# Optimization experiments

Hardware: AMD Instinct MI355X
Metric: run time of the kernel (lower is better)

Reference implementation:

```python
import jax, jax.numpy as jnp
import numpy as np

B, S, H, D = 4, 2048, 16, 64
E = H * D  # embedding_dim = 1024


def setup_inputs() -> dict:
    key = jax.random.key(0)
    ks = jax.random.split(key, 5)
    scale = 1.0 / np.sqrt(E)
    return {
        "x": jax.random.normal(ks[0], (B, S, E), dtype=jnp.float32),
        "wq": jax.random.normal(ks[1], (E, E), dtype=jnp.float32) * scale,
        "wk": jax.random.normal(ks[2], (E, E), dtype=jnp.float32) * scale,
        "wv": jax.random.normal(ks[3], (E, E), dtype=jnp.float32) * scale,
        "wo": jax.random.normal(ks[4], (E, E), dtype=jnp.float32) * scale,
    }


def reference(x, wq, wk, wv, wo):
    b, s, e = x.shape
    # nn.Linear: y = x @ W^T (no bias; use_bias=False)
    q = (x @ wq.T).reshape(b, s, H, D)
    k = (x @ wk.T).reshape(b, s, H, D)
    v = (x @ wv.T).reshape(b, s, H, D)
    # NOTE: original scales by sqrt(embedding_dim), not sqrt(head_dim)
    scores = jnp.einsum("bqhd,bkhd->bhqk", q, k) / jnp.sqrt(jnp.float32(e))
    causal = jnp.tril(jnp.ones((s, s), dtype=bool))  # mask[:s,:s]
    scores = jnp.where(causal, scores, -jnp.inf)
    attn = jax.nn.softmax(scores, axis=-1)
    out = jnp.einsum("bhql,blhd->bqhd", attn, v).reshape(b, s, e)
    return out @ wo.T
```

## Files before the change

### kernel.cpp

```cpp
#include <hip/hip_runtime.h>
#include <hip/hip_bf16.h>

#define E_DIM 1024
#define NHEAD 16
#define HDIM  64
#define BATCH 4
#define SEQ   2048
#define RQKV  (3 * E_DIM)

typedef __attribute__((ext_vector_type(8))) short bf16x8;
typedef __attribute__((ext_vector_type(4))) float f32x4;
typedef __attribute__((ext_vector_type(16))) float f32x16;

#define SCL2 0.04508422f

static __device__ __forceinline__ unsigned short bits_of(__hip_bfloat16 h) {
    return *reinterpret_cast<unsigned short*>(&h);
}

static __device__ __forceinline__ void gload_lds16(const void* g, void* l) {
    __builtin_amdgcn_global_load_lds(
        (__attribute__((address_space(1))) void*)g,
        (__attribute__((address_space(3))) void*)l, 16, 0, 0);
}

static __device__ __forceinline__ unsigned cvt_pk_bf16(float a, float b) {
    unsigned r;
    asm("v_cvt_pk_bf16_f32 %0, %1, %2" : "=v"(r) : "v"(a), "v"(b));
    return r;
}

static __device__ __forceinline__ float exp2_raw(float x) {
    float r;
    asm("v_exp_f32 %0, %1" : "=v"(r) : "v"(x));
    return r;
}

__global__ void cast_all_kernel(
    const float* __restrict__ x,  const float* __restrict__ wq,
    const float* __restrict__ wk, const float* __restrict__ wv,
    const float* __restrict__ wo,
    __hip_bfloat16* __restrict__ xb, __hip_bfloat16* __restrict__ wqkvb,
    __hip_bfloat16* __restrict__ wob) {
    const int NX4 = (BATCH * SEQ * E_DIM) / 4;
    const int NW4 = (E_DIM * E_DIM) / 4;
    int id = blockIdx.x * 256 + threadIdx.x;

    const float* in;
    __hip_bfloat16* out;
    float scl = 1.0f;
    if (id < NX4) {
        in = x; out = xb;
    } else {
        const int r = id - NX4;
        const int wsel = r >> 18;
        id = r & (NW4 - 1);
        switch (wsel) {
            case 0: in = wq; out = wqkvb;            scl = SCL2; break;
            case 1: in = wk; out = wqkvb + NW4 * 4;  break;
            case 2: in = wv; out = wqkvb + NW4 * 8;  break;
            default: in = wo; out = wob;             break;
        }
    }
    float4 v = reinterpret_cast<const float4*>(in)[id];
    ushort4 u;
    u.x = bits_of(__float2bfloat16(v.x * scl));
    u.y = bits_of(__float2bfloat16(v.y * scl));
    u.z = bits_of(__float2bfloat16(v.z * scl));
    u.w = bits_of(__float2bfloat16(v.w * scl));
    reinterpret_cast<ushort4*>(out)[id] = u;
}

template<int FN, int OUT_F32>
__global__ __launch_bounds__(512) void gemm_ph(
    const __hip_bfloat16* __restrict__ A,
    const __hip_bfloat16* __restrict__ Bw,
    void* __restrict__ Cv,
    int M, int N, int K) {
    constexpr int BN = FN * 64;
    __shared__ __align__(16) __hip_bfloat16 As[2][128 * 64];
    __shared__ __align__(16) __hip_bfloat16 Bs[2][BN * 64];

    const int nbx = gridDim.x;
    const int lin = blockIdx.y * nbx + blockIdx.x;
    const int cpx = (nbx * gridDim.y) >> 3;
    const int swz = (lin & 7) * cpx + (lin >> 3);
    const int mBase = (swz / nbx) * 128, nBase = (swz % nbx) * BN;

    const int t = threadIdx.x, lane = t & 63, w = t >> 6;
    const int wr = w >> 2, wc = w & 3;
    const int lr = lane & 15;
    const int lkb = (lane >> 4) * 16;

    f32x4 acc[4][FN];
#pragma unroll
    for (int i = 0; i < 4; ++i)
#pragma unroll
        for (int j = 0; j < FN; ++j) acc[i][j] = (f32x4){0.f, 0.f, 0.f, 0.f};

    const int NKT = K >> 6;

    auto STAGE = [&](int kt, int b) {
#pragma unroll
        for (int i = 0; i < 2; ++i) {
            const int q = i * 512 + t;
            const int r = q >> 3, cb = (q & 7) * 16;
            const char* src = (const char*)A +
                ((size_t)(mBase + r) * K + kt * 64) * 2 + (cb ^ ((r & 7) << 4));
            gload_lds16(src, (char*)&As[b][0] + q * 16);
        }
#pragma unroll
        for (int i = 0; i < FN; ++i) {
            const int q = i * 512 + t;
            const int r = q >> 3, cb = (q & 7) * 16;
            const char* src = (const char*)Bw +
                ((size_t)(nBase + r) * K + kt * 64) * 2 + (cb ^ ((r & 7) << 4));
            gload_lds16(src, (char*)&Bs[b][0] + q * 16);
        }
    };

    STAGE(0, 0);
    for (int kt = 0; kt < NKT; ++kt) {
        const int buf = kt & 1;
        asm volatile("s_waitcnt vmcnt(0)" ::: "memory");
        __builtin_amdgcn_s_barrier();
        __builtin_amdgcn_sched_barrier(0);

        bf16x8 bfr[FN][2];
        {
#pragma unroll
            for (int fn = 0; fn < FN; ++fn)
#pragma unroll
                for (int ks = 0; ks < 2; ++ks) {
                    const int R = wc * (FN * 16) + fn * 16 + lr;
                    const int addr = R * 128 + ((ks * 64 + lkb) ^ ((R & 7) << 4));
                    bfr[fn][ks] = *reinterpret_cast<const bf16x8*>(
                        (const char*)&Bs[buf][0] + addr);
                }
            bf16x8 af[2][2];
#pragma unroll
            for (int f = 0; f < 2; ++f)
#pragma unroll
                for (int ks = 0; ks < 2; ++ks) {
                    const int R = wr * 64 + f * 16 + lr;
                    const int addr = R * 128 + ((ks * 64 + lkb) ^ ((R & 7) << 4));
                    af[f][ks] = *reinterpret_cast<const bf16x8*>(
                        (const char*)&As[buf][0] + addr);
                }
            if (kt + 1 < NKT) STAGE(kt + 1, buf ^ 1);
            asm volatile("s_waitcnt lgkmcnt(0)" ::: "memory");
            __builtin_amdgcn_sched_barrier(0);
            __builtin_amdgcn_s_setprio(1);
#pragma unroll
            for (int f = 0; f < 2; ++f)
#pragma unroll
                for (int fn = 0; fn < FN; ++fn)
#pragma unroll
                    for (int ks = 0; ks < 2; ++ks)
                        acc[f][fn] = __builtin_amdgcn_mfma_f32_16x16x32_bf16(
                            af[f][ks], bfr[fn][ks], acc[f][fn], 0, 0, 0);
            __builtin_amdgcn_s_setprio(0);
            __builtin_amdgcn_s_barrier();
        }
        {
            bf16x8 af[2][2];
#pragma unroll
            for (int f = 0; f < 2; ++f)
#pragma unroll
                for (int ks = 0; ks < 2; ++ks) {
                    const int R = wr * 64 + (f + 2) * 16 + lr;
                    const int addr = R * 128 + ((ks * 64 + lkb) ^ ((R & 7) << 4));
                    af[f][ks] = *reinterpret_cast<const bf16x8*>(
                        (const char*)&As[buf][0] + addr);
                }
            asm volatile("s_waitcnt lgkmcnt(0)" ::: "memory");
            __builtin_amdgcn_sched_barrier(0);
            __builtin_amdgcn_s_setprio(1);
#pragma unroll
            for (int f = 0; f < 2; ++f)
#pragma unroll
                for (int fn = 0; fn < FN; ++fn)
#pragma unroll
                    for (int ks = 0; ks < 2; ++ks)
                        acc[f + 2][fn] = __builtin_amdgcn_mfma_f32_16x16x32_bf16(
                            af[f][ks], bfr[fn][ks], acc[f + 2][fn], 0, 0, 0);
            __builtin_amdgcn_s_setprio(0);
        }
    }

#pragma unroll
    for (int fm = 0; fm < 4; ++fm)
#pragma unroll
        for (int fn = 0; fn < FN; ++fn)
#pragma unroll
            for (int v = 0; v < 4; ++v) {
                const int row = mBase + wr * 64 + fm * 16 + (lane >> 4) * 4 + v;
                const int col = nBase + wc * (FN * 16) + fn * 16 + lr;
                if (OUT_F32)
                    ((float*)Cv)[(size_t)row * N + col] = acc[fm][fn][v];
                else
                    ((__hip_bfloat16*)Cv)[(size_t)row * N + col] =
                        __float2bfloat16(acc[fm][fn][v]);
            }
}

__global__ __launch_bounds__(256) void attn_kernel(
    const __hip_bfloat16* __restrict__ QKV,
    __hip_bfloat16* __restrict__ O) {
    __shared__ __align__(16) __hip_bfloat16 Kl[2][64][64];
    __shared__ __align__(16) __hip_bfloat16 Vt[2][64][64];

    const int t = threadIdx.x, w = t >> 6, lane = t & 63;
    const int lq = lane & 31, hi = lane >> 5;

    const int id = blockIdx.x;
    const int c = id & 7, k = id >> 3;
    const int bh = (k & 7) * 8 + c;
    const int qq = k >> 3;
    const int qb = (qq & 4) ? (qq < 8 ? qq + 4 : qq - 12) : 15 - qq;
    const int b = bh >> 4, h = bh & 15;

    const size_t rb = (size_t)b * SEQ;
    const __hip_bfloat16* Qg = QKV + rb * RQKV + h * HDIM;
    const __hip_bfloat16* Kg = QKV + rb * RQKV + E_DIM + h * HDIM;
    const __hip_bfloat16* Vg = QKV + rb * RQKV + 2 * E_DIM + h * HDIM;

    const int kst_row  = w * 16 + (lane >> 3);
    const int kst_slot = lane & 7;
    const int vkp = t & 31, vd0 = (t >> 5) * 8;

    const int qw0 = qb * 128 + w * 32;
    const int qg  = qw0 + lq;

    bf16x8 aq[4];
#pragma unroll
    for (int d0 = 0; d0 < 4; ++d0)
        aq[d0] = *reinterpret_cast<const bf16x8*>(
            Qg + (size_t)qg * RQKV + d0 * 16 + hi * 8);

    f32x16 oa[2];
#pragma unroll
    for (int m = 0; m < 2; ++m)
#pragma unroll
        for (int r = 0; r < 16; ++r) oa[m][r] = 0.f;
    float l_run = 0.f;

    const int NP = qb + 1;
    for (int pr = 0; pr < NP; ++pr) {
        const int k0a = pr * 128;
        __syncthreads();

#pragma unroll
        for (int half = 0; half < 2; ++half)
#pragma unroll
            for (int i = 0; i < 2; ++i) {
                const int r = kst_row + i * 8;
                const char* src =
                    (const char*)(Kg + (size_t)(k0a + half * 64 + r) * RQKV) +
                    ((kst_slot * 16) ^ ((r & 7) << 4));
                gload_lds16(src, &Kl[half][w * 16 + i * 8][0]);
            }
        {
            const __hip_bfloat16* vp0 =
                Vg + (size_t)(k0a + 2 * vkp) * RQKV + vd0;
            const __hip_bfloat16* vp1 = vp0 + (size_t)64 * RQKV;
            union { bf16x8 v; unsigned u[4]; } A0, B0, A1, B1;
            A0.v = *reinterpret_cast<const bf16x8*>(vp0);
            B0.v = *reinterpret_cast<const bf16x8*>(vp0 + RQKV);
            A1.v = *reinterpret_cast<const bf16x8*>(vp1);
            B1.v = *reinterpret_cast<const bf16x8*>(vp1 + RQKV);
            char* vt0 = reinterpret_cast<char*>(&Vt[0][0][0]);
            char* vt1 = reinterpret_cast<char*>(&Vt[1][0][0]);
#pragma unroll
            for (int jw = 0; jw < 4; ++jw) {
                const int da = vd0 + 2 * jw, db = da + 1;
                const int offa = da * 128 + ((vkp * 4) ^ ((da & 7) << 4));
                const int offb = db * 128 + ((vkp * 4) ^ ((db & 7) << 4));
                *reinterpret_cast<unsigned*>(vt0 + offa) =
                    __builtin_amdgcn_perm(B0.u[jw], A0.u[jw], 0x05040100u);
                *reinterpret_cast<unsigned*>(vt0 + offb) =
                    __builtin_amdgcn_perm(B0.u[jw], A0.u[jw], 0x07060302u);
                *reinterpret_cast<unsigned*>(vt1 + offa) =
                    __builtin_amdgcn_perm(B1.u[jw], A1.u[jw], 0x05040100u);
                *reinterpret_cast<unsigned*>(vt1 + offb) =
                    __builtin_amdgcn_perm(B1.u[jw], A1.u[jw], 0x07060302u);
            }
        }
        __syncthreads();

#pragma unroll
        for (int half = 0; half < 2; ++half) {
            const int k0 = k0a + half * 64;
            if (k0 > qw0 + 31) continue;

            f32x16 sc2[2];
            const char* klbase = (const char*)&Kl[half][0][0];
#pragma unroll
            for (int tt = 0; tt < 2; ++tt) {
#pragma unroll
                for (int r = 0; r < 16; ++r) sc2[tt][r] = 0.f;
                const int kr = tt * 32 + lq;
                const char* kbase = klbase + kr * 128;
                const int swz = (kr & 7) << 4;
#pragma unroll
                for (int d0 = 0; d0 < 4; ++d0) {
                    bf16x8 ak = *reinterpret_cast<const bf16x8*>(
                        kbase + ((d0 * 32 + hi * 16) ^ swz));
                    sc2[tt] = __builtin_amdgcn_mfma_f32_32x32x16_bf16(
                        ak, aq[d0], sc2[tt], 0, 0, 0);
                }
            }
            if (k0 + 63 > qw0) {
#pragma unroll
                for (int tt = 0; tt < 2; ++tt)
#pragma unroll
                    for (int r = 0; r < 16; ++r) {
                        const int kgl = k0 + tt * 32 +
                                        (r & 3) + 8 * (r >> 2) + 4 * hi;
                        if (kgl > qg) sc2[tt][r] = -1e30f;
                    }
            }
            float rsum = 0.f;
#pragma unroll
            for (int tt = 0; tt < 2; ++tt) {
                float s0 = 0.f, s1 = 0.f, s2 = 0.f, s3 = 0.f;
#pragma unroll
                for (int r = 0; r < 16; r += 4) {
                    float p0 = exp2_raw(sc2[tt][r]);
                    float p1 = exp2_raw(sc2[tt][r + 1]);
                    float p2 = exp2_raw(sc2[tt][r + 2]);
                    float p3 = exp2_raw(sc2[tt][r + 3]);
                    sc2[tt][r] = p0; sc2[tt][r + 1] = p1;
                    sc2[tt][r + 2] = p2; sc2[tt][r + 3] = p3;
                    s0 += p0; s1 += p1; s2 += p2; s3 += p3;
                }
                rsum += (s0 + s1) + (s2 + s3);
            }
            rsum += __shfl_xor(rsum, 32);
            l_run += rsum;

            const char* vtbase = (const char*)&Vt[half][0][0];
#pragma unroll
            for (int tt = 0; tt < 2; ++tt)
#pragma unroll
                for (int sl = 0; sl < 2; ++sl) {
                    const int rbs = sl * 8;
                    const unsigned wA = cvt_pk_bf16(sc2[tt][rbs + 0], sc2[tt][rbs + 1]);
                    const unsigned wB = cvt_pk_bf16(sc2[tt][rbs + 2], sc2[tt][rbs + 3]);
                    const unsigned wC = cvt_pk_bf16(sc2[tt][rbs + 4], sc2[tt][rbs + 5]);
                    const unsigned wD = cvt_pk_bf16(sc2[tt][rbs + 6], sc2[tt][rbs + 7]);
                    const auto pA = __builtin_amdgcn_permlane32_swap(wA, wC, false, false);
                    const auto pB = __builtin_amdgcn_permlane32_swap(wB, wD, false, false);
                    union { unsigned u[4]; bf16x8 v; } pf;
                    pf.u[0] = pA[0]; pf.u[1] = pB[0];
                    pf.u[2] = pA[1]; pf.u[3] = pB[1];
                    const int ks = tt * 2 + sl;
#pragma unroll
                    for (int m = 0; m < 2; ++m) {
                        const int dr = m * 32 + lq;
                        bf16x8 av = *reinterpret_cast<const bf16x8*>(
                            vtbase + dr * 128 +
                            ((ks * 32 + hi * 16) ^ ((dr & 7) << 4)));
                        oa[m] = __builtin_amdgcn_mfma_f32_32x32x16_bf16(
                            av, pf.v, oa[m], 0, 0, 0);
                    }
                }
        }
    }

    const float inv = 1.f / l_run;
    __hip_bfloat16* Orow = O + (rb + qg) * E_DIM + h * HDIM;
#pragma unroll
    for (int m = 0; m < 2; ++m)
#pragma unroll
        for (int q4 = 0; q4 < 4; ++q4) {
            ushort4 pk;
            pk.x = bits_of(__float2bfloat16(oa[m][q4 * 4 + 0] * inv));
            pk.y = bits_of(__float2bfloat16(oa[m][q4 * 4 + 1] * inv));
            pk.z = bits_of(__float2bfloat16(oa[m][q4 * 4 + 2] * inv));
            pk.w = bits_of(__float2bfloat16(oa[m][q4 * 4 + 3] * inv));
            *reinterpret_cast<ushort4*>(Orow + m * 32 + q4 * 8 + 4 * hi) = pk;
        }
}

extern "C" void kernel_launch(void* const* d_in, const int* in_sizes, int n_in,
                              void* d_out, int out_size, void* d_ws, size_t ws_size,
                              hipStream_t stream) {
    const float* x  = (const float*)d_in[0];
    const float* wq = (const float*)d_in[1];
    const float* wk = (const float*)d_in[2];
    const float* wv = (const float*)d_in[3];
    const float* wo = (const float*)d_in[4];

    const size_t SZ_X = (size_t)BATCH * SEQ * E_DIM;
    const size_t SZ_W = (size_t)E_DIM * E_DIM;

    char* p = (char*)d_ws;
    __hip_bfloat16* xb    = (__hip_bfloat16*)p; p += SZ_X * 2;
    __hip_bfloat16* wqkvb = (__hip_bfloat16*)p; p += 3 * SZ_W * 2;
    __hip_bfloat16* wob   = (__hip_bfloat16*)p; p += SZ_W * 2;
    __hip_bfloat16* QKVb  = (__hip_bfloat16*)p; p += SZ_X * 3 * 2;
    __hip_bfloat16* attb  = (__hip_bfloat16*)p; p += SZ_X * 2;

    cast_all_kernel<<<dim3(12288), 256, 0, stream>>>(
        x, wq, wk, wv, wo, xb, wqkvb, wob);

    const int M = BATCH * SEQ;
    gemm_ph<3, 0><<<dim3(RQKV / 192, M / 128), 512, 0, stream>>>(
        xb, wqkvb, QKVb, M, RQKV, E_DIM);

    attn_kernel<<<dim3(1024), 256, 0, stream>>>(QKVb, attb);

    gemm_ph<2, 1><<<dim3(E_DIM / 128, M / 128), 512, 0, stream>>>(
        attb, wob, d_out, M, E_DIM, E_DIM);
}
```

Measured before the change: 151.7 us.

## Split long causal query blocks across two KV halves and combine partials

Query tiles 8–15, which have the longest causal KV ranges, are each split into two work items. Each item covers half of the KV pairs and writes unnormalized fp32 partial outputs and row sums to workspace. A new combine kernel adds the two partials, normalizes, and writes bf16. This is meant to shorten the longest blocks and improve load balance across the grid. The cost is an extra kernel launch plus roughly 33 MB of fp32 partials written and read back. The plain summing of partials relies on softmax using no running max.

```diff
diff --git a/kernel.cpp b/kernel.cpp
--- a/kernel.cpp
+++ b/kernel.cpp
@@ -206,7 +206,9 @@
 
 __global__ __launch_bounds__(256) void attn_kernel(
     const __hip_bfloat16* __restrict__ QKV,
-    __hip_bfloat16* __restrict__ O) {
+    __hip_bfloat16* __restrict__ O,
+    float* __restrict__ Po,
+    float* __restrict__ Pl) {
     __shared__ __align__(16) __hip_bfloat16 Kl[2][64][64];
     __shared__ __align__(16) __hip_bfloat16 Vt[2][64][64];
 
@@ -214,11 +216,23 @@
     const int lq = lane & 31, hi = lane >> 5;
 
     const int id = blockIdx.x;
-    const int c = id & 7, k = id >> 3;
-    const int bh = (k & 7) * 8 + c;
-    const int qq = k >> 3;
-    const int qb = (qq & 4) ? (qq < 8 ? qq + 4 : qq - 12) : 15 - qq;
+    const int c = id & 7, j = id >> 3;
+    const int bh = (j & 7) * 8 + c;
+    const int job = j >> 3;
     const int b = bh >> 4, h = bh & 15;
+
+    int qb, prS, prE, sIdx = 0;
+    const bool split = (job >= 8);
+    if (!split) {
+        qb = job; prS = 0; prE = qb + 1;
+    } else {
+        const int qt = (job - 8) >> 1;
+        sIdx = (job - 8) & 1;
+        qb = 8 + qt;
+        const int h0 = (qb + 2) >> 1;
+        prS = sIdx ? h0 : 0;
+        prE = sIdx ? qb + 1 : h0;
+    }
 
     const size_t rb = (size_t)b * SEQ;
     const __hip_bfloat16* Qg = QKV + rb * RQKV + h * HDIM;
@@ -245,8 +259,7 @@
         for (int r = 0; r < 16; ++r) oa[m][r] = 0.f;
     float l_run = 0.f;
 
-    const int NP = qb + 1;
-    for (int pr = 0; pr < NP; ++pr) {
+    for (int pr = prS; pr < prE; ++pr) {
         const int k0a = pr * 128;
         __syncthreads();
 
@@ -368,19 +381,72 @@
         }
     }
 
-    const float inv = 1.f / l_run;
-    __hip_bfloat16* Orow = O + (rb + qg) * E_DIM + h * HDIM;
-#pragma unroll
-    for (int m = 0; m < 2; ++m)
-#pragma unroll
-        for (int q4 = 0; q4 < 4; ++q4) {
-            ushort4 pk;
-            pk.x = bits_of(__float2bfloat16(oa[m][q4 * 4 + 0] * inv));
-            pk.y = bits_of(__float2bfloat16(oa[m][q4 * 4 + 1] * inv));
-            pk.z = bits_of(__float2bfloat16(oa[m][q4 * 4 + 2] * inv));
-            pk.w = bits_of(__float2bfloat16(oa[m][q4 * 4 + 3] * inv));
-            *reinterpret_cast<ushort4*>(Orow + m * 32 + q4 * 8 + 4 * hi) = pk;
-        }
+    if (!split) {
+        const float inv = 1.f / l_run;
+        __hip_bfloat16* Orow = O + (rb + qg) * E_DIM + h * HDIM;
+#pragma unroll
+        for (int m = 0; m < 2; ++m)
+#pragma unroll
+            for (int q4 = 0; q4 < 4; ++q4) {
+                ushort4 pk;
+                pk.x = bits_of(__float2bfloat16(oa[m][q4 * 4 + 0] * inv));
+                pk.y = bits_of(__float2bfloat16(oa[m][q4 * 4 + 1] * inv));
+                pk.z = bits_of(__float2bfloat16(oa[m][q4 * 4 + 2] * inv));
+                pk.w = bits_of(__float2bfloat16(oa[m][q4 * 4 + 3] * inv));
+                *reinterpret_cast<ushort4*>(Orow + m * 32 + q4 * 8 + 4 * hi) = pk;
+            }
+    } else {
+        const int bhqt = bh * 8 + (qb - 8);
+        const int qlocal = w * 32 + lq;
+        float* Pr = Po + ((size_t)(bhqt * 2 + sIdx) * 128 + qlocal) * 64;
+#pragma unroll
+        for (int m = 0; m < 2; ++m)
+#pragma unroll
+            for (int q4 = 0; q4 < 4; ++q4) {
+                float4 st = {oa[m][q4 * 4 + 0], oa[m][q4 * 4 + 1],
+                             oa[m][q4 * 4 + 2], oa[m][q4 * 4 + 3]};
+                *reinterpret_cast<float4*>(Pr + m * 32 + q4 * 8 + 4 * hi) = st;
+            }
+        if (hi == 0)
+            Pl[(size_t)bhqt * 256 + sIdx * 128 + qlocal] = l_run;
+    }
+}
+
+__global__ __launch_bounds__(256) void combine_kernel(
+    const float* __restrict__ Po, const float* __restrict__ Pl,
+    __hip_bfloat16* __restrict__ O) {
+    const int g = blockIdx.x * 256 + threadIdx.x;
+    const int row = g >> 3, oct = g & 7;
+    const int ql = row & 127, bhqt = row >> 7;
+    const int qt = bhqt & 7, bh = bhqt >> 3;
+    const int b = bh >> 4, h = bh & 15;
+    const int qb = 8 + qt;
+
+    const float l = Pl[(size_t)bhqt * 256 + ql] +
+                    Pl[(size_t)bhqt * 256 + 128 + ql];
+    const float inv = 1.f / l;
+
+    const size_t a0 = ((size_t)(bhqt * 2) * 128 + ql) * 64 + oct * 8;
+    const size_t a1 = a0 + 128 * 64;
+    const float4 p0a = *reinterpret_cast<const float4*>(Po + a0);
+    const float4 p0b = *reinterpret_cast<const float4*>(Po + a0 + 4);
+    const float4 p1a = *reinterpret_cast<const float4*>(Po + a1);
+    const float4 p1b = *reinterpret_cast<const float4*>(Po + a1 + 4);
+
+    ushort4 u0, u1;
+    u0.x = bits_of(__float2bfloat16((p0a.x + p1a.x) * inv));
+    u0.y = bits_of(__float2bfloat16((p0a.y + p1a.y) * inv));
+    u0.z = bits_of(__float2bfloat16((p0a.z + p1a.z) * inv));
+    u0.w = bits_of(__float2bfloat16((p0a.w + p1a.w) * inv));
+    u1.x = bits_of(__float2bfloat16((p0b.x + p1b.x) * inv));
+    u1.y = bits_of(__float2bfloat16((p0b.y + p1b.y) * inv));
+    u1.z = bits_of(__float2bfloat16((p0b.z + p1b.z) * inv));
+    u1.w = bits_of(__float2bfloat16((p0b.w + p1b.w) * inv));
+
+    __hip_bfloat16* dst = O + ((size_t)b * SEQ + qb * 128 + ql) * E_DIM +
+                          h * HDIM + oct * 8;
+    *reinterpret_cast<ushort4*>(dst) = u0;
+    *reinterpret_cast<ushort4*>(dst + 4) = u1;
 }
 
 extern "C" void kernel_launch(void* const* d_in, const int* in_sizes, int n_in,
@@ -401,6 +467,8 @@
     __hip_bfloat16* wob   = (__hip_bfloat16*)p; p += SZ_W * 2;
     __hip_bfloat16* QKVb  = (__hip_bfloat16*)p; p += SZ_X * 3 * 2;
     __hip_bfloat16* attb  = (__hip_bfloat16*)p; p += SZ_X * 2;
+    float* Po = (float*)p; p += (size_t)512 * 2 * 128 * 64 * 4;
+    float* Pl = (float*)p; p += (size_t)512 * 256 * 4;
 
     cast_all_kernel<<<dim3(12288), 256, 0, stream>>>(
         x, wq, wk, wv, wo, xb, wqkvb, wob);
@@ -409,7 +477,8 @@
     gemm_ph<3, 0><<<dim3(RQKV / 192, M / 128), 512, 0, stream>>>(
         xb, wqkvb, QKVb, M, RQKV, E_DIM);
 
-    attn_kernel<<<dim3(1024), 256, 0, stream>>>(QKVb, attb);
+    attn_kernel<<<dim3(1536), 256, 0, stream>>>(QKVb, attb, Po, Pl);
+    combine_kernel<<<dim3(2048), 256, 0, stream>>>(Po, Pl, attb);
 
     gemm_ph<2, 1><<<dim3(E_DIM / 128, M / 128), 512, 0, stream>>>(
         attb, wob, d_out, M, E_DIM, E_DIM);
```

Result: slower. 168.5 us (+11.1%).
